# Optimization experiments

Hardware: AMD Instinct MI355X
Metric: run time of the kernel (lower is better)

## Reference

```python
import jax, jax.numpy as jnp
import numpy as np

DIM = 1024
NUM_HEADS = 16
HEAD_DIM = DIM // NUM_HEADS
B, S = 2, 2048


def setup_inputs() -> dict:
    key = jax.random.key(0)
    ks = jax.random.split(key, 7)
    x = jax.random.normal(ks[0], (B, S, DIM), dtype=jnp.float32)
    cos = jax.random.uniform(ks[1], (S, HEAD_DIM // 2), dtype=jnp.float32)
    sin = jax.random.uniform(ks[2], (S, HEAD_DIM // 2), dtype=jnp.float32)
    scale = 1.0 / np.sqrt(DIM)
    Wq = jax.random.normal(ks[3], (DIM, DIM), dtype=jnp.float32) * scale
    Wk = jax.random.normal(ks[4], (DIM, DIM), dtype=jnp.float32) * scale
    Wv = jax.random.normal(ks[5], (DIM, DIM), dtype=jnp.float32) * scale
    Wo = jax.random.normal(ks[6], (DIM, DIM), dtype=jnp.float32) * scale
    return {"x": x, "cos": cos, "sin": sin, "Wq": Wq, "Wk": Wk, "Wv": Wv, "Wo": Wo}


def _apply_rope(t, c, s):
    # t: [B, S, H, hd]; c, s: [1, S, 1, hd] (already doubled)
    half = t.shape[-1] // 2
    t1, t2 = t[..., :half], t[..., half:]
    rot = jnp.concatenate([-t2, t1], axis=-1)
    return t * c + rot * s


def reference(x, cos, sin, Wq, Wk, Wv, Wo):
    Bs, Ss, D = x.shape
    H, hd = NUM_HEADS, HEAD_DIM
    q = (x @ Wq).reshape(Bs, Ss, H, hd)
    k = (x @ Wk).reshape(Bs, Ss, H, hd)
    v = (x @ Wv).reshape(Bs, Ss, H, hd)
    # repeat(1,1,1,2) in torch tiles cos as [cos, cos] along last dim
    c = jnp.concatenate([cos, cos], axis=-1)[None, :, None, :]
    s = jnp.concatenate([sin, sin], axis=-1)[None, :, None, :]
    q = _apply_rope(q, c, s)
    k = _apply_rope(k, c, s)
    # SDPA, non-causal, scale 1/sqrt(hd)
    scores = jnp.einsum("bqhd,bkhd->bhqk", q, k) / jnp.sqrt(jnp.float32(hd))
    attn = jax.nn.softmax(scores, axis=-1)
    out = jnp.einsum("bhqk,bkhd->bqhd", attn, v).reshape(Bs, Ss, D)
    return out @ Wo
```

## Files before the change

kernel.cpp:

```cpp
#include <hip/hip_runtime.h>

#define B_  2
#define S_  2048
#define D_  1024
#define H_  16
#define HD_ 64
#define M_  (B_*S_)

typedef __bf16 bf16x8 __attribute__((ext_vector_type(8)));
typedef float  f32x4  __attribute__((ext_vector_type(4)));
typedef float  f32x16 __attribute__((ext_vector_type(16)));
typedef unsigned short ushort_t;

static __device__ __forceinline__ ushort_t f2bf(float f) {
  __bf16 b = (__bf16)f;
  return __builtin_bit_cast(ushort_t, b);
}
static __device__ __forceinline__ float bf2f(ushort_t u) {
  return (float)__builtin_bit_cast(__bf16, u);
}

typedef __attribute__((address_space(1))) const unsigned u32g;
typedef __attribute__((address_space(3))) unsigned u32l;
static __device__ __forceinline__ void gll16(const ushort_t* g, __bf16* l) {
  __builtin_amdgcn_global_load_lds((u32g*)g, (u32l*)l, 16, 0, 0);
}

__global__ __launch_bounds__(256) void convert_x(const float* __restrict__ x,
                                                 ushort_t* __restrict__ xb) {
  size_t e = ((size_t)blockIdx.x * 256 + threadIdx.x) * 8;
  float4 a = *(const float4*)(x + e);
  float4 b = *(const float4*)(x + e + 4);
  uint4 pk;
  pk.x = (unsigned)f2bf(a.x) | ((unsigned)f2bf(a.y) << 16);
  pk.y = (unsigned)f2bf(a.z) | ((unsigned)f2bf(a.w) << 16);
  pk.z = (unsigned)f2bf(b.x) | ((unsigned)f2bf(b.y) << 16);
  pk.w = (unsigned)f2bf(b.z) | ((unsigned)f2bf(b.w) << 16);
  *(uint4*)(xb + e) = pk;
}

__global__ __launch_bounds__(256) void transpose_w(const float* __restrict__ Wq,
                                                   const float* __restrict__ Wk,
                                                   const float* __restrict__ Wv,
                                                   const float* __restrict__ Wo,
                                                   ushort_t* __restrict__ Wqkvt,
                                                   ushort_t* __restrict__ Wot) {
  __shared__ __bf16 T[64][72];
  const int z = blockIdx.z;
  const float* W = (z == 0) ? Wq : (z == 1) ? Wk : (z == 2) ? Wv : Wo;
  ushort_t* Wt = (z < 3) ? (Wqkvt + (size_t)z * 1048576) : Wot;
  const int k0 = blockIdx.y * 64, n0 = blockIdx.x * 64;
  const int t = threadIdx.x, r = t >> 2, c16 = (t & 3) * 16;
#pragma unroll
  for (int i = 0; i < 4; i++) {
    float4 v = *(const float4*)(W + (size_t)(k0 + r) * D_ + n0 + c16 + i * 4);
    T[r][c16 + i*4 + 0] = (__bf16)v.x;
    T[r][c16 + i*4 + 1] = (__bf16)v.y;
    T[r][c16 + i*4 + 2] = (__bf16)v.z;
    T[r][c16 + i*4 + 3] = (__bf16)v.w;
  }
  __syncthreads();
  ushort_t vals[16];
#pragma unroll
  for (int i = 0; i < 16; i++) vals[i] = __builtin_bit_cast(ushort_t, T[c16 + i][r]);
  ushort_t* dst = Wt + (size_t)(n0 + r) * D_ + k0 + c16;
  *(uint4*)dst       = *(const uint4*)&vals[0];
  *(uint4*)(dst + 8) = *(const uint4*)&vals[8];
}

__global__ __launch_bounds__(256) void transpose_v(const ushort_t* __restrict__ Vb,
                                                   ushort_t* __restrict__ Vtg) {
  __shared__ __bf16 T[64][72];
  const int bh = blockIdx.y, kt = blockIdx.x;
  const int t = threadIdx.x, r = t >> 2, c16 = (t & 3) * 16;
  const ushort_t* src = Vb + ((size_t)bh * S_ + kt*64 + r) * 64 + c16;
  *(uint4*)&T[r][c16]     = *(const uint4*)src;
  *(uint4*)&T[r][c16 + 8] = *(const uint4*)(src + 8);
  __syncthreads();
  ushort_t vals[16];
#pragma unroll
  for (int i = 0; i < 16; i++) {
    int c = c16 + i;
    int k = ((c & 1) << 5) | (c >> 1);
    vals[i] = __builtin_bit_cast(ushort_t, T[k][r]);
  }
  ushort_t* dst = Vtg + ((size_t)bh * 64 + r) * S_ + kt*64 + c16;
  *(uint4*)dst       = *(const uint4*)&vals[0];
  *(uint4*)(dst + 8) = *(const uint4*)&vals[8];
}

template<int OMODE, int BS>
__global__ __launch_bounds__(256) void gemm_bf16(const ushort_t* __restrict__ Wt,
                                                 const ushort_t* __restrict__ X,
                                                 void* __restrict__ Cp,
                                                 const float* __restrict__ cosb,
                                                 const float* __restrict__ sinb) {
  constexpr int NT = BS / 32;
  constexpr int SM = (OMODE == 1) ? 16384 : 6144;
  __shared__ __bf16 SMEM[SM];
  __bf16* As = SMEM;
  __bf16* Bs = SMEM + 4096;
  const int t = threadIdx.x, w = t >> 6, lane = t & 63, l15 = lane & 15, g = lane >> 4;
  const int wr = w >> 1, wc = w & 1;
  const int f0 = blockIdx.y * 128, s0 = blockIdx.x * BS;
  const int al = lane >> 2, ac = (lane & 3) * 8;
  f32x4 acc[4][NT] = {};

  for (int k0 = 0; k0 < D_; k0 += 32) {
    __syncthreads();
#pragma unroll
    for (int i = 0; i < 2; i++)
      gll16(Wt + (size_t)(f0 + i*64 + w*16 + al) * D_ + k0 + ac, &As[i*2048 + w*512]);
#pragma unroll
    for (int i = 0; i < BS/64; i++)
      gll16(X + (size_t)(s0 + i*64 + w*16 + al) * D_ + k0 + ac, &Bs[i*2048 + w*512]);
    __syncthreads();
    bf16x8 af[4], bfv[NT];
#pragma unroll
    for (int mt = 0; mt < 4; mt++)  af[mt]  = *(const bf16x8*)&As[(wr*64 + mt*16 + l15)*32 + g*8];
#pragma unroll
    for (int nt = 0; nt < NT; nt++) bfv[nt] = *(const bf16x8*)&Bs[(wc*(BS/2) + nt*16 + l15)*32 + g*8];
#pragma unroll
    for (int mt = 0; mt < 4; mt++)
#pragma unroll
      for (int nt = 0; nt < NT; nt++)
        acc[mt][nt] = __builtin_amdgcn_mfma_f32_16x16x32_bf16(af[mt], bfv[nt], acc[mt][nt], 0, 0, 0);
  }

  if (OMODE == 0) {
#pragma unroll
    for (int mt = 0; mt < 4; mt++)
#pragma unroll
      for (int nt = 0; nt < NT; nt++) {
        int s = s0 + wc*(BS/2) + nt*16 + l15;
        int f = f0 + wr*64 + mt*16 + g*4;
        *(float4*)&((float*)Cp)[(size_t)s * D_ + f] = *(float4*)&acc[mt][nt];
      }
  } else {
    const int hid = blockIdx.y*2 + wr;
    const int mat = hid >> 4, h = hid & 15;
    const int s0w = s0 + wc*64;
    ushort_t* dst = (ushort_t*)Cp + (size_t)mat * 4194304;
    const float QS = 0.125f * 1.4426950408889634f;
    if (mat < 2) {
#pragma unroll
      for (int mt = 0; mt < 2; mt++)
#pragma unroll
        for (int nt = 0; nt < 4; nt++) {
          int s  = s0w + nt*16 + l15;
          int sq = s & (S_ - 1);
          float4 c4 = *(const float4*)&cosb[sq*32 + mt*16 + g*4];
          float4 s4 = *(const float4*)&sinb[sq*32 + mt*16 + g*4];
          const float* cf = (const float*)&c4;
          const float* sf = (const float*)&s4;
#pragma unroll
          for (int r = 0; r < 4; r++) {
            float v1 = acc[mt][nt][r], v2 = acc[mt+2][nt][r];
            float r1 = v1*cf[r] - v2*sf[r];
            float r2 = v2*cf[r] + v1*sf[r];
            if (mat == 0) { r1 *= QS; r2 *= QS; }
            acc[mt][nt][r] = r1; acc[mt+2][nt][r] = r2;
          }
        }
    }
    __syncthreads();
    __bf16* Tw = SMEM + w*4096;
#pragma unroll
    for (int mt = 0; mt < 4; mt++)
#pragma unroll
      for (int nt = 0; nt < 4; nt++) {
        int s_loc = nt*16 + l15;
        int d0 = mt*16 + g*4;
        int ch = (d0 >> 3) ^ (s_loc & 7);
        ushort_t pk[4];
#pragma unroll
        for (int r = 0; r < 4; r++) pk[r] = f2bf(acc[mt][nt][r]);
        *(ushort4*)&Tw[s_loc*64 + ch*8 + (d0 & 7)] = *(const ushort4*)pk;
      }
#pragma unroll
    for (int j = 0; j < 8; j++) {
      int s_loc = j*8 + (lane >> 3);
      int ci = lane & 7;
      int ch = ci ^ (s_loc & 7);
      uint4 v = *(const uint4*)&Tw[s_loc*64 + ch*8];
      int s = s0w + s_loc;
      int b = s >> 11, srow = s & (S_ - 1);
      *(uint4*)&dst[(((size_t)(b*H_ + h) * S_ + srow) << 6) + ci*8] = v;
    }
  }
}

__global__ __launch_bounds__(256) void attn32(const ushort_t* __restrict__ Q,
                                              const ushort_t* __restrict__ K,
                                              const ushort_t* __restrict__ Vtg,
                                              ushort_t* __restrict__ op0,
                                              ushort_t* __restrict__ op1,
                                              float* __restrict__ lw) {
  __shared__ __bf16 KsL[2][64 * 64];
  __shared__ __bf16 VtL[2][64 * 64];
  __shared__ __bf16 Ps[4][32][72];
  const int t = threadIdx.x, w = t >> 6, lane = t & 63;
  const int l31 = lane & 31, h2 = lane >> 5, sw = l31 & 7;
  const int bh = blockIdx.y, q0 = blockIdx.x * 128 + w * 32, z = blockIdx.z;

  const ushort_t* Qp = Q + ((size_t)bh * S_ + q0 + l31) * HD_;
  bf16x8 qf[4];
#pragma unroll
  for (int kc = 0; kc < 4; kc++) qf[kc] = *(const bf16x8*)(Qp + kc*16 + h2*8);

  f32x16 o0 = {}, o1 = {};
  float lp[16];
#pragma unroll
  for (int i = 0; i < 16; i++) lp[i] = 0.f;

  const ushort_t* Kb = K   + ((size_t)bh * S_ + z * 1024) * HD_;
  const ushort_t* Vg = Vtg + (size_t)bh * HD_ * S_ + z * 1024;
  const int krl = lane >> 3;
  const int kco = ((lane & 7) ^ krl) * 8;

  asm volatile("s_waitcnt vmcnt(0)" ::: "memory");

#define STAGE(KT, CB)                                                        \
  {                                                                          \
    _Pragma("unroll")                                                        \
    for (int p = 0; p < 2; p++) {                                            \
      int bk = w*8 + p*32;                                                   \
      gll16(Kb + (size_t)((KT)*64 + bk + krl) * HD_ + kco, &KsL[CB][bk*64]); \
    }                                                                        \
    _Pragma("unroll")                                                        \
    for (int p = 0; p < 2; p++) {                                            \
      int bd = w*8 + p*32;                                                   \
      gll16(Vg + (size_t)(bd + krl) * S_ + (KT)*64 + kco, &VtL[CB][bd*64]);  \
    }                                                                        \
  }

  STAGE(0, 0);
  for (int kt = 0; kt < 16; kt++) {
    const int cur = kt & 1;
    if (kt < 15) {
      STAGE(kt + 1, cur ^ 1);
      asm volatile("s_waitcnt vmcnt(4)" ::: "memory");
    } else {
      asm volatile("s_waitcnt vmcnt(0)" ::: "memory");
    }
    asm volatile("s_barrier" ::: "memory");

    f32x16 s0 = {}, s1 = {};
#pragma unroll
    for (int kc = 0; kc < 4; kc++) {
      int cs = ((kc*2 + h2) ^ sw) * 8;
      bf16x8 b0 = *(const bf16x8*)&KsL[cur][l31*64 + cs];
      bf16x8 b1 = *(const bf16x8*)&KsL[cur][(32 + l31)*64 + cs];
      s0 = __builtin_amdgcn_mfma_f32_32x32x16_bf16(qf[kc], b0, s0, 0, 0, 0);
      s1 = __builtin_amdgcn_mfma_f32_32x32x16_bf16(qf[kc], b1, s1, 0, 0, 0);
    }

#pragma unroll
    for (int i = 0; i < 16; i++) {
      float p0 = __builtin_amdgcn_exp2f(s0[i]);
      float p1 = __builtin_amdgcn_exp2f(s1[i]);
      lp[i] += p0 + p1;
      int row = (i & 3) + 8*(i >> 2) + 4*h2;
      unsigned pk = (unsigned)f2bf(p0) | ((unsigned)f2bf(p1) << 16);
      *(unsigned*)&Ps[w][row][2*l31] = pk;
    }

#pragma unroll
    for (int kc = 0; kc < 4; kc++) {
      int cs = ((kc*2 + h2) ^ sw) * 8;
      bf16x8 pf = *(const bf16x8*)&Ps[w][l31][kc*16 + h2*8];
      bf16x8 v0 = *(const bf16x8*)&VtL[cur][l31*64 + cs];
      bf16x8 v1 = *(const bf16x8*)&VtL[cur][(32 + l31)*64 + cs];
      o0 = __builtin_amdgcn_mfma_f32_32x32x16_bf16(pf, v0, o0, 0, 0, 0);
      o1 = __builtin_amdgcn_mfma_f32_32x32x16_bf16(pf, v1, o1, 0, 0, 0);
    }

    asm volatile("s_barrier" ::: "memory");
  }
#undef STAGE

#pragma unroll
  for (int i = 0; i < 16; i++) {
#pragma unroll
    for (int mk = 1; mk < 32; mk <<= 1) lp[i] += __shfl_xor(lp[i], mk, 64);
  }

  ushort_t* op = (z == 0) ? op0 : op1;
  float* lwp = lw + (size_t)(z*32 + bh) * S_;
#pragma unroll
  for (int i = 0; i < 16; i++) {
    int row = q0 + (i & 3) + 8*(i >> 2) + 4*h2;
    size_t base = ((size_t)bh * S_ + row) * 64;
    op[base + l31]      = f2bf(o0[i]);
    op[base + 32 + l31] = f2bf(o1[i]);
    if (l31 == 0) lwp[row] = lp[i];
  }
}

__global__ __launch_bounds__(256) void combine(const ushort_t* __restrict__ op0,
                                               const ushort_t* __restrict__ op1,
                                               const float* __restrict__ lw,
                                               ushort_t* __restrict__ att) {
  int tid = blockIdx.x * 256 + threadIdx.x;
  int d8 = (tid & 7) * 8;
  int s  = (tid >> 3) & (S_ - 1);
  int bh = tid >> 14;
  size_t pb = ((size_t)bh * S_ + s) * 64 + d8;
  uint4 a = *(const uint4*)(op0 + pb);
  uint4 b = *(const uint4*)(op1 + pb);
  float inv = 1.f / (lw[(size_t)bh * S_ + s] + lw[(size_t)(32 + bh) * S_ + s]);
  const ushort_t* as = (const ushort_t*)&a;
  const ushort_t* bs = (const ushort_t*)&b;
  ushort_t outv[8];
#pragma unroll
  for (int i = 0; i < 8; i++)
    outv[i] = f2bf((bf2f(as[i]) + bf2f(bs[i])) * inv);
  int bidx = bh >> 4, h = bh & 15;
  *(uint4*)(att + ((size_t)(bidx * S_ + s)) * D_ + h*64 + d8) = *(const uint4*)outv;
}

extern "C" void kernel_launch(void* const* d_in, const int* in_sizes, int n_in,
                              void* d_out, int out_size, void* d_ws, size_t ws_size,
                              hipStream_t stream) {
  (void)in_sizes; (void)n_in; (void)out_size; (void)ws_size;
  const float* x    = (const float*)d_in[0];
  const float* cosb = (const float*)d_in[1];
  const float* sinb = (const float*)d_in[2];
  const float* Wq   = (const float*)d_in[3];
  const float* Wk   = (const float*)d_in[4];
  const float* Wv   = (const float*)d_in[5];
  const float* Wo   = (const float*)d_in[6];
  float* out = (float*)d_out;

  ushort_t* w     = (ushort_t*)d_ws;
  ushort_t* xb    = w;
  ushort_t* Wqkvt = w + 4194304;
  ushort_t* Wot   = w + 7340032;
  ushort_t* Qb    = w + 8388608;
  ushort_t* Kb    = w + 12582912;
  ushort_t* Vb    = w + 16777216;
  ushort_t* Vtg   = w + 20971520;
  ushort_t* att   = w + 25165824;
  float*    lw    = (float*)Wqkvt;

  convert_x<<<2048, 256, 0, stream>>>(x, xb);
  transpose_w<<<dim3(16, 16, 4), 256, 0, stream>>>(Wq, Wk, Wv, Wo, Wqkvt, Wot);

  gemm_bf16<1,128><<<dim3(32, 24), 256, 0, stream>>>(Wqkvt, xb, Qb, cosb, sinb);

  transpose_v<<<dim3(32, 32), 256, 0, stream>>>(Vb, Vtg);

  attn32<<<dim3(16, 32, 2), 256, 0, stream>>>(Qb, Kb, Vtg, xb, Vb, lw);

  combine<<<2048, 256, 0, stream>>>(xb, Vb, lw, att);

  gemm_bf16<0,64><<<dim3(64, 8), 256, 0, stream>>>(Wot, att, out, nullptr, nullptr);
}
```

Before: 229.0 us.

## Process two 32-row query subtiles per wave to reuse K/V fragments

Each wave in the attention kernel now handles 64 query rows, as two 32-row subtiles, instead of 32. K and V fragments are loaded from LDS into registers once per key tile and reused across both subtiles, which halves LDS reads per MFMA and halves the K/V global staging per query. The grid is halved to match. In exchange it uses more registers and a larger P buffer in LDS, which may reduce occupancy, and the smaller grid leaves fewer blocks to fill the CUs.

```diff
diff --git a/kernel.cpp b/kernel.cpp
--- a/kernel.cpp
+++ b/kernel.cpp
@@ -198,20 +198,24 @@
                                               float* __restrict__ lw) {
   __shared__ __bf16 KsL[2][64 * 64];
   __shared__ __bf16 VtL[2][64 * 64];
-  __shared__ __bf16 Ps[4][32][72];
+  __shared__ __bf16 Ps[4][64 * 64];
   const int t = threadIdx.x, w = t >> 6, lane = t & 63;
   const int l31 = lane & 31, h2 = lane >> 5, sw = l31 & 7;
-  const int bh = blockIdx.y, q0 = blockIdx.x * 128 + w * 32, z = blockIdx.z;
-
-  const ushort_t* Qp = Q + ((size_t)bh * S_ + q0 + l31) * HD_;
-  bf16x8 qf[4];
-#pragma unroll
-  for (int kc = 0; kc < 4; kc++) qf[kc] = *(const bf16x8*)(Qp + kc*16 + h2*8);
-
-  f32x16 o0 = {}, o1 = {};
-  float lp[16];
-#pragma unroll
-  for (int i = 0; i < 16; i++) lp[i] = 0.f;
+  const int bh = blockIdx.y, q0 = blockIdx.x * 256 + w * 64, z = blockIdx.z;
+
+  bf16x8 qf[8];
+#pragma unroll
+  for (int qs = 0; qs < 2; qs++)
+#pragma unroll
+    for (int kc = 0; kc < 4; kc++)
+      qf[qs*4 + kc] = *(const bf16x8*)(Q + ((size_t)bh * S_ + q0 + qs*32 + l31) * HD_ + kc*16 + h2*8);
+
+  f32x16 o[4] = {};
+  float lp[2][16];
+#pragma unroll
+  for (int qs = 0; qs < 2; qs++)
+#pragma unroll
+    for (int i = 0; i < 16; i++) lp[qs][i] = 0.f;
 
   const ushort_t* Kb = K   + ((size_t)bh * S_ + z * 1024) * HD_;
   const ushort_t* Vg = Vtg + (size_t)bh * HD_ * S_ + z * 1024;
@@ -245,56 +249,73 @@
     }
     asm volatile("s_barrier" ::: "memory");
 
-    f32x16 s0 = {}, s1 = {};
-#pragma unroll
-    for (int kc = 0; kc < 4; kc++) {
-      int cs = ((kc*2 + h2) ^ sw) * 8;
-      bf16x8 b0 = *(const bf16x8*)&KsL[cur][l31*64 + cs];
-      bf16x8 b1 = *(const bf16x8*)&KsL[cur][(32 + l31)*64 + cs];
-      s0 = __builtin_amdgcn_mfma_f32_32x32x16_bf16(qf[kc], b0, s0, 0, 0, 0);
-      s1 = __builtin_amdgcn_mfma_f32_32x32x16_bf16(qf[kc], b1, s1, 0, 0, 0);
-    }
-
+    bf16x8 kf[8];
+#pragma unroll
+    for (int ks = 0; ks < 2; ks++)
+#pragma unroll
+      for (int kc = 0; kc < 4; kc++)
+        kf[ks*4 + kc] = *(const bf16x8*)&KsL[cur][(ks*32 + l31)*64 + ((kc*2 + h2) ^ sw)*8];
+
+#pragma unroll
+    for (int qs = 0; qs < 2; qs++) {
+      f32x16 s0 = {}, s1 = {};
+#pragma unroll
+      for (int kc = 0; kc < 4; kc++) {
+        s0 = __builtin_amdgcn_mfma_f32_32x32x16_bf16(qf[qs*4 + kc], kf[kc],     s0, 0, 0, 0);
+        s1 = __builtin_amdgcn_mfma_f32_32x32x16_bf16(qf[qs*4 + kc], kf[4 + kc], s1, 0, 0, 0);
+      }
+#pragma unroll
+      for (int i = 0; i < 16; i++) {
+        float p0 = __builtin_amdgcn_exp2f(s0[i]);
+        float p1 = __builtin_amdgcn_exp2f(s1[i]);
+        lp[qs][i] += p0 + p1;
+        int row = qs*32 + (i & 3) + 8*(i >> 2) + 4*h2;
+        unsigned pk = (unsigned)f2bf(p0) | ((unsigned)f2bf(p1) << 16);
+        *(unsigned*)&Ps[w][row*64 + 2*l31] = pk;
+      }
+    }
+
+    bf16x8 vf[8];
+#pragma unroll
+    for (int ds = 0; ds < 2; ds++)
+#pragma unroll
+      for (int kc = 0; kc < 4; kc++)
+        vf[ds*4 + kc] = *(const bf16x8*)&VtL[cur][(ds*32 + l31)*64 + ((kc*2 + h2) ^ sw)*8];
+
+#pragma unroll
+    for (int qs = 0; qs < 2; qs++) {
+#pragma unroll
+      for (int kc = 0; kc < 4; kc++) {
+        bf16x8 pf = *(const bf16x8*)&Ps[w][(qs*32 + l31)*64 + kc*16 + h2*8];
+        o[qs*2]     = __builtin_amdgcn_mfma_f32_32x32x16_bf16(pf, vf[kc],     o[qs*2],     0, 0, 0);
+        o[qs*2 + 1] = __builtin_amdgcn_mfma_f32_32x32x16_bf16(pf, vf[4 + kc], o[qs*2 + 1], 0, 0, 0);
+      }
+    }
+
+    asm volatile("s_barrier" ::: "memory");
+  }
+#undef STAGE
+
+#pragma unroll
+  for (int qs = 0; qs < 2; qs++)
 #pragma unroll
     for (int i = 0; i < 16; i++) {
-      float p0 = __builtin_amdgcn_exp2f(s0[i]);
-      float p1 = __builtin_amdgcn_exp2f(s1[i]);
-      lp[i] += p0 + p1;
-      int row = (i & 3) + 8*(i >> 2) + 4*h2;
-      unsigned pk = (unsigned)f2bf(p0) | ((unsigned)f2bf(p1) << 16);
-      *(unsigned*)&Ps[w][row][2*l31] = pk;
-    }
-
-#pragma unroll
-    for (int kc = 0; kc < 4; kc++) {
-      int cs = ((kc*2 + h2) ^ sw) * 8;
-      bf16x8 pf = *(const bf16x8*)&Ps[w][l31][kc*16 + h2*8];
-      bf16x8 v0 = *(const bf16x8*)&VtL[cur][l31*64 + cs];
-      bf16x8 v1 = *(const bf16x8*)&VtL[cur][(32 + l31)*64 + cs];
-      o0 = __builtin_amdgcn_mfma_f32_32x32x16_bf16(pf, v0, o0, 0, 0, 0);
-      o1 = __builtin_amdgcn_mfma_f32_32x32x16_bf16(pf, v1, o1, 0, 0, 0);
-    }
-
-    asm volatile("s_barrier" ::: "memory");
-  }
-#undef STAGE
-
-#pragma unroll
-  for (int i = 0; i < 16; i++) {
-#pragma unroll
-    for (int mk = 1; mk < 32; mk <<= 1) lp[i] += __shfl_xor(lp[i], mk, 64);
-  }
+#pragma unroll
+      for (int mk = 1; mk < 32; mk <<= 1) lp[qs][i] += __shfl_xor(lp[qs][i], mk, 64);
+    }
 
   ushort_t* op = (z == 0) ? op0 : op1;
   float* lwp = lw + (size_t)(z*32 + bh) * S_;
 #pragma unroll
-  for (int i = 0; i < 16; i++) {
-    int row = q0 + (i & 3) + 8*(i >> 2) + 4*h2;
-    size_t base = ((size_t)bh * S_ + row) * 64;
-    op[base + l31]      = f2bf(o0[i]);
-    op[base + 32 + l31] = f2bf(o1[i]);
-    if (l31 == 0) lwp[row] = lp[i];
-  }
+  for (int qs = 0; qs < 2; qs++)
+#pragma unroll
+    for (int i = 0; i < 16; i++) {
+      int row = q0 + qs*32 + (i & 3) + 8*(i >> 2) + 4*h2;
+      size_t base = ((size_t)bh * S_ + row) * 64;
+      op[base + l31]      = f2bf(o[qs*2][i]);
+      op[base + 32 + l31] = f2bf(o[qs*2 + 1][i]);
+      if (l31 == 0) lwp[row] = lp[qs][i];
+    }
 }
 
 __global__ __launch_bounds__(256) void combine(const ushort_t* __restrict__ op0,
@@ -350,7 +371,7 @@
 
   transpose_v<<<dim3(32, 32), 256, 0, stream>>>(Vb, Vtg);
 
-  attn32<<<dim3(16, 32, 2), 256, 0, stream>>>(Qb, Kb, Vtg, xb, Vb, lw);
+  attn32<<<dim3(8, 32, 2), 256, 0, stream>>>(Qb, Kb, Vtg, xb, Vb, lw);
 
   combine<<<2048, 256, 0, stream>>>(xb, Vb, lw, att);
 
```

Result: slower. 249.8 us (+9.1%).
